# Performance work log

Measured on AMD Instinct MI355X. Metric: run time of the kernel, lower is better.

The kernel has to match this reference:

```python
import jax, jax.numpy as jnp
import numpy as np

B, T, D, NH, L = 8192, 100, 44, 64, 8  # batch, seq/ode steps, obs_dim, rnn hidden, latent


def setup_inputs() -> dict:
    key = jax.random.key(0)
    ks = jax.random.split(key, 12)
    s = 0.1
    return {
        "x": jax.random.normal(ks[0], (B, T, D), jnp.float32),
        "mask": jax.random.randint(ks[1], (B, T, D), 0, 2).astype(jnp.float32),
        "epsilon": jax.random.normal(ks[2], (B, L), jnp.float32),
        "Wi2h": jax.random.normal(ks[3], (D + NH, NH), jnp.float32) * s,
        "bi2h": jnp.zeros((NH,), jnp.float32),
        "Wh2o": jax.random.normal(ks[4], (NH, 2 * L), jnp.float32) * s,
        "bh2o": jnp.zeros((2 * L,), jnp.float32),
        "Wf1": jax.random.normal(ks[5], (L, NH), jnp.float32) * s,
        "bf1": jnp.zeros((NH,), jnp.float32),
        "Wf2": jax.random.normal(ks[6], (NH, NH), jnp.float32) * s,
        "bf2": jnp.zeros((NH,), jnp.float32),
        "Wf3": jax.random.normal(ks[7], (NH, L), jnp.float32) * s,
        "bf3": jnp.zeros((L,), jnp.float32),
        "Wd1": jax.random.normal(ks[8], (L, NH), jnp.float32) * s,
        "bd1": jnp.zeros((NH,), jnp.float32),
        "Wd2": jax.random.normal(ks[9], (NH, D), jnp.float32) * s,
        "bd2": jnp.zeros((D,), jnp.float32),
    }


def reference(x, mask, epsilon, Wi2h, bi2h, Wh2o, bh2o,
              Wf1, bf1, Wf2, bf2, Wf3, bf3, Wd1, bd1, Wd2, bd2):
    masked_x = x * mask  # [B,T,D]

    # --- reverse-time recognition RNN (scan over time, reversed) ---
    def rnn_step(h, obs):
        h = jnp.tanh(jnp.concatenate([obs, h], axis=1) @ Wi2h + bi2h)
        return h, None

    xs_rev = jnp.transpose(masked_x[:, ::-1, :], (1, 0, 2))  # [T,B,D]
    h0 = jnp.zeros((x.shape[0], Wi2h.shape[1]), x.dtype)
    h_final, _ = jax.lax.scan(rnn_step, h0, xs_rev)
    out = h_final @ Wh2o + bh2o  # [B,2L]
    qz0_mean, qz0_logvar = out[:, :L], out[:, L:]

    # reparameterized latent sample
    z0 = epsilon * jnp.exp(0.5 * qz0_logvar) + qz0_mean  # [B,L]

    # --- latent ODE dynamics, fixed-step RK4 over ts = linspace(0,1,100) ---
    def f(z):
        h1 = jax.nn.elu(z @ Wf1 + bf1)
        h2 = jax.nn.elu(h1 @ Wf2 + bf2)
        return h2 @ Wf3 + bf3

    dt = jnp.asarray(1.0 / (T - 1), x.dtype)

    def rk4_step(z, _):
        k1 = f(z)
        k2 = f(z + 0.5 * dt * k1)
        k3 = f(z + 0.5 * dt * k2)
        k4 = f(z + dt * k3)
        zn = z + (dt / 6.0) * (k1 + 2.0 * k2 + 2.0 * k3 + k4)
        return zn, zn

    _, zs = jax.lax.scan(rk4_step, z0, None, length=T - 1)  # [T-1,B,L]
    pred_z = jnp.transpose(jnp.concatenate([z0[None], zs], axis=0), (1, 0, 2))  # [B,T,L]

    # --- decoder ---
    pred_x = jax.nn.relu(pred_z @ Wd1 + bd1) @ Wd2 + bd2  # [B,T,D]

    # fill observed entries back in
    updated_x = jnp.where(masked_x != 0, masked_x, pred_x)

    # --- loss ---
    noise_logvar = 2.0 * jnp.log(jnp.asarray(0.3, x.dtype))
    log2pi = jnp.log(jnp.asarray(2.0 * np.pi, x.dtype))
    logpx = (-0.5 * (log2pi + noise_logvar +
                     (x - updated_x) ** 2 / jnp.exp(noise_logvar))).sum((-1, -2))  # [B]
    kl = (-0.5 * qz0_logvar + (jnp.exp(qz0_logvar) + qz0_mean ** 2) / 2.0 - 0.5).sum(-1)  # [B]
    loss = jnp.mean(-logpx + kl)
    return loss
```

## Files before the change

kernel.cpp:

```cpp
#include <hip/hip_runtime.h>
#include <stdint.h>


constexpr int B_ = 8192, T_ = 100, D_ = 44, NH_ = 64, L_ = 8;

typedef __bf16 bf16x8 __attribute__((ext_vector_type(8)));
typedef float f32x4 __attribute__((ext_vector_type(4)));
typedef uint32_t u32x4 __attribute__((ext_vector_type(4)));
typedef uint32_t u32x2 __attribute__((ext_vector_type(2)));

__device__ __forceinline__ float fexp2(float x) { return __builtin_amdgcn_exp2f(x); }
__device__ __forceinline__ float frcp(float x) { return __builtin_amdgcn_rcpf(x); }
__device__ __forceinline__ float fexp(float x) { return fexp2(x * 1.44269504088896341f); }
__device__ __forceinline__ float tanh_f(float x) {
  float e = fexp2(x * 2.88539008177792681f);
  return 1.0f - 2.0f * frcp(e + 1.0f);
}
__device__ __forceinline__ float elu_f(float x) { return x > 0.0f ? x : (fexp(x) - 1.0f); }
__device__ __forceinline__ uint32_t f2bs(float x) {
  return (uint32_t)__builtin_bit_cast(unsigned short, (__bf16)x);
}
__device__ __forceinline__ uint32_t pk(float lo, float hi) { return f2bs(lo) | (f2bs(hi) << 16); }
__device__ __forceinline__ uint32_t sh(uint32_t v, int s) { return (uint32_t)__shfl((int)v, s, 64); }
__device__ __forceinline__ f32x4 mfma16(bf16x8 a, bf16x8 b, f32x4 c) {
  return __builtin_amdgcn_mfma_f32_16x16x32_bf16(a, b, c, 0, 0, 0);
}
__device__ __forceinline__ bf16x8 pack8(float a, float b, float c, float d,
                                        float e, float f, float g, float h) {
  u32x4 u = {pk(a, b), pk(c, d), pk(e, f), pk(g, h)};
  return __builtin_bit_cast(bf16x8, u);
}
__device__ __forceinline__ float f4get(const float4& f, int i) {
  return i == 0 ? f.x : (i == 1 ? f.y : (i == 2 ? f.z : f.w));
}

__device__ __forceinline__ void repack_lds(uint32_t* tb, int c, int q,
                                           const f32x4* e, bf16x8* bh) {
#pragma unroll
  for (int tau = 0; tau < 4; ++tau) {
    u32x2 w = {pk(e[tau][0], e[tau][1]), pk(e[tau][2], e[tau][3])};
    *(u32x2*)(tb + 36 * c + 8 * tau + 2 * q) = w;
  }
#pragma unroll
  for (int ks = 0; ks < 2; ++ks) {
    u32x4 r = *(const u32x4*)(tb + 36 * c + 16 * ks + 4 * q);
    bh[ks] = __builtin_bit_cast(bf16x8, r);
  }
}

__device__ __forceinline__ bf16x8 build_bz(f32x4 z, int c, int q) {
  uint32_t p01 = pk(z[0], z[1]), p23 = pk(z[2], z[3]);
  u32x4 u = {sh(p01, c), sh(p23, c), sh(p01, c + 16), sh(p23, c + 16)};
  if (q == 1) u[0] = 0x3f80u;
  return __builtin_bit_cast(bf16x8, u);
}

__global__ __launch_bounds__(64) void fused_kernel(
    const float* __restrict__ x, const float* __restrict__ mask,
    const float* __restrict__ eps,
    const float* __restrict__ Wi2h, const float* __restrict__ bi2h,
    const float* __restrict__ Wh2o, const float* __restrict__ bh2o,
    const float* __restrict__ Wf1, const float* __restrict__ bf1,
    const float* __restrict__ Wf2, const float* __restrict__ bf2,
    const float* __restrict__ Wf3, const float* __restrict__ bf3,
    const float* __restrict__ Wd1, const float* __restrict__ bd1,
    const float* __restrict__ Wd2, const float* __restrict__ bd2,
    float* __restrict__ part) {
  const int lane = threadIdx.x;
  const int c = lane & 15, q = lane >> 4;
  const int r0 = blockIdx.x * 16;

  __shared__ uint32_t tbufA[576];
  __shared__ uint32_t tbufB[576];

  bf16x8 Ai[4][4];
#pragma unroll
  for (int tau = 0; tau < 4; ++tau)
#pragma unroll
    for (int ks = 0; ks < 4; ++ks) {
      bf16x8 f;
      const int m = 16 * tau + c;
#pragma unroll
      for (int i = 0; i < 8; ++i) {
        const int k = 32 * ks + 8 * q + i;
        float v = 0.0f;
        if (k < 64) v = Wi2h[(44 + k) * 64 + m];
        else if (k < 108) v = Wi2h[(k - 64) * 64 + m];
        else if (k == 108) v = bi2h[m];
        f[i] = (__bf16)v;
      }
      Ai[tau][ks] = f;
    }
  bf16x8 Ah2o[2];
#pragma unroll
  for (int ks = 0; ks < 2; ++ks) {
    bf16x8 f;
#pragma unroll
    for (int i = 0; i < 8; ++i) f[i] = (__bf16)Wh2o[(32 * ks + 8 * q + i) * 16 + c];
    Ah2o[ks] = f;
  }
  f32x4 bo;
#pragma unroll
  for (int r = 0; r < 4; ++r) bo[r] = bh2o[4 * q + r];

  const float* xrowbase = x + (size_t)(r0 + c) * T_ * D_;
  const float* mrowbase = mask + (size_t)(r0 + c) * T_ * D_;

  auto load_obs = [&](int t, float4& a0, float4& a1, float4& b0, float4& b1,
                      float4& ma0, float4& ma1, float4& mb0, float4& mb1) {
    const float4* xr = (const float4*)(xrowbase + (size_t)t * D_);
    const float4* mr = (const float4*)(mrowbase + (size_t)t * D_);
    a0 = xr[2 * q]; a1 = xr[2 * q + 1]; ma0 = mr[2 * q]; ma1 = mr[2 * q + 1];
    float4 zz = {0.f, 0.f, 0.f, 0.f};
    b0 = zz; b1 = zz; mb0 = zz; mb1 = zz;
    if (q == 0) { b0 = xr[8]; b1 = xr[9]; mb0 = mr[8]; mb1 = mr[9]; }
    else if (q == 1) { b0 = xr[10]; mb0 = mr[10]; }
  };

  f32x4 hc[4] = {};
  float4 a0, a1, b0, b1, ma0, ma1, mb0, mb1;
  load_obs(T_ - 1, a0, a1, b0, b1, ma0, ma1, mb0, mb1);

#pragma unroll 1
  for (int s = 0; s < T_; ++s) {
    const int t = T_ - 1 - s;
    float4 ca0 = a0, ca1 = a1, cb0 = b0, cb1 = b1;
    float4 cm0 = ma0, cm1 = ma1, cn0 = mb0, cn1 = mb1;
    if (t > 0) load_obs(t - 1, a0, a1, b0, b1, ma0, ma1, mb0, mb1);

    bf16x8 bh[2];
    repack_lds(tbufA, c, q, hc, bh);
    bf16x8 o2 = pack8(ca0.x * cm0.x, ca0.y * cm0.y, ca0.z * cm0.z, ca0.w * cm0.w,
                      ca1.x * cm1.x, ca1.y * cm1.y, ca1.z * cm1.z, ca1.w * cm1.w);
    const float e44 = (q == 1) ? 1.0f : cb1.x * cn1.x;
    bf16x8 o3 = pack8(cb0.x * cn0.x, cb0.y * cn0.y, cb0.z * cn0.z, cb0.w * cn0.w,
                      e44, cb1.y * cn1.y, cb1.z * cn1.z, cb1.w * cn1.w);
#pragma unroll
    for (int tau = 0; tau < 4; ++tau) {
      f32x4 zero = {0.f, 0.f, 0.f, 0.f};
      f32x4 acc = mfma16(Ai[tau][0], bh[0], zero);
      acc = mfma16(Ai[tau][1], bh[1], acc);
      acc = mfma16(Ai[tau][2], o2, acc);
      acc = mfma16(Ai[tau][3], o3, acc);
#pragma unroll
      for (int r = 0; r < 4; ++r) hc[tau][r] = tanh_f(acc[r]);
    }
  }

  bf16x8 bhF[2];
  repack_lds(tbufA, c, q, hc, bhF);
  f32x4 o = mfma16(Ah2o[1], bhF[1], mfma16(Ah2o[0], bhF[0], bo));

  float lv[4];
#pragma unroll
  for (int r = 0; r < 4; ++r)
    lv[r] = __int_as_float(__shfl(__float_as_int(o[r]), lane + 32, 64));

  float klt = 0.0f;
  f32x4 z = {};
  if (q < 2) {
    const float4 ev = *(const float4*)(eps + (size_t)(r0 + c) * 8 + 4 * q);
#pragma unroll
    for (int r = 0; r < 4; ++r) {
      const float m = o[r];
      z[r] = f4get(ev, r) * fexp(0.5f * lv[r]) + m;
      klt += -0.5f * lv[r] + (fexp(lv[r]) + m * m) * 0.5f - 0.5f;
    }
  }
  klt += __shfl_xor(klt, 1);  klt += __shfl_xor(klt, 2);
  klt += __shfl_xor(klt, 4);  klt += __shfl_xor(klt, 8);
  klt += __shfl_xor(klt, 16); klt += __shfl_xor(klt, 32);

  __builtin_amdgcn_sched_barrier(0);

  bf16x8 A1[4], A2[4][2], A3[2], Ad1[4], Ad2[3][2];
#pragma unroll
  for (int tau = 0; tau < 4; ++tau) {
    bf16x8 f1, fd;
#pragma unroll
    for (int i = 0; i < 8; ++i) {
      const int k = 8 * q + i;
      f1[i] = (__bf16)(k < 8 ? Wf1[k * 64 + 16 * tau + c] : (k == 8 ? bf1[16 * tau + c] : 0.0f));
      fd[i] = (__bf16)(k < 8 ? Wd1[k * 64 + 16 * tau + c] : (k == 8 ? bd1[16 * tau + c] : 0.0f));
    }
    A1[tau] = f1; Ad1[tau] = fd;
#pragma unroll
    for (int ks = 0; ks < 2; ++ks) {
      bf16x8 g;
#pragma unroll
      for (int i = 0; i < 8; ++i) g[i] = (__bf16)Wf2[(32 * ks + 8 * q + i) * 64 + 16 * tau + c];
      A2[tau][ks] = g;
    }
  }
#pragma unroll
  for (int ks = 0; ks < 2; ++ks) {
    bf16x8 f;
#pragma unroll
    for (int i = 0; i < 8; ++i)
      f[i] = (__bf16)((c < 8) ? Wf3[(32 * ks + 8 * q + i) * 8 + c] : 0.0f);
    A3[ks] = f;
  }
#pragma unroll
  for (int tau = 0; tau < 3; ++tau)
#pragma unroll
    for (int ks = 0; ks < 2; ++ks) {
      bf16x8 f;
      const int m = 16 * tau + c;
#pragma unroll
      for (int i = 0; i < 8; ++i)
        f[i] = (__bf16)((m < 44) ? Wd2[(32 * ks + 8 * q + i) * 44 + m] : 0.0f);
      Ad2[tau][ks] = f;
    }
  f32x4 b2_[4], b3_, bd2_[3];
#pragma unroll
  for (int tau = 0; tau < 4; ++tau)
#pragma unroll
    for (int r = 0; r < 4; ++r) b2_[tau][r] = bf2[16 * tau + 4 * q + r];
#pragma unroll
  for (int r = 0; r < 4; ++r) b3_[r] = (q < 2) ? bf3[4 * q + r] : 0.0f;
#pragma unroll
  for (int tau = 0; tau < 3; ++tau)
#pragma unroll
    for (int r = 0; r < 4; ++r) {
      const int d = 16 * tau + 4 * q + r;
      bd2_[tau][r] = (d < 44) ? bd2[d] : 0.0f;
    }

  auto feval = [&](bf16x8 bz) -> f32x4 {
    f32x4 h[4];
#pragma unroll
    for (int tau = 0; tau < 4; ++tau) {
      f32x4 zero = {0.f, 0.f, 0.f, 0.f};
      h[tau] = mfma16(A1[tau], bz, zero);
#pragma unroll
      for (int r = 0; r < 4; ++r) h[tau][r] = elu_f(h[tau][r]);
    }
    bf16x8 bh[2];
    repack_lds(tbufA, c, q, h, bh);
    f32x4 g[4];
#pragma unroll
    for (int tau = 0; tau < 4; ++tau) {
      g[tau] = mfma16(A2[tau][1], bh[1], mfma16(A2[tau][0], bh[0], b2_[tau]));
#pragma unroll
      for (int r = 0; r < 4; ++r) g[tau][r] = elu_f(g[tau][r]);
    }
    bf16x8 bg[2];
    repack_lds(tbufA, c, q, g, bg);
    return mfma16(A3[1], bg[1], mfma16(A3[0], bg[0], b3_));
  };

  auto load_xm = [&](int t, float4* xv, float4* mv) {
#pragma unroll
    for (int tau = 0; tau < 3; ++tau) {
      const int d0 = 16 * tau + 4 * q;
      if (d0 < 44) {
        const size_t off = (size_t)(r0 + c) * T_ * D_ + (size_t)t * D_ + d0;
        xv[tau] = *(const float4*)(x + off);
        mv[tau] = *(const float4*)(mask + off);
      }
    }
  };

  const float dt = 1.0f / (float)(T_ - 1);
  const float hdt = 0.5f * dt;
  float qacc = 0.0f;

  float4 xc[3], mc[3], xn[3], mn[3];
  load_xm(0, xc, mc);

#pragma unroll 1
  for (int t = 0; t < T_; ++t) {
    if (t < T_ - 1) load_xm(t + 1, xn, mn);

    bf16x8 bz = build_bz(z, c, q);

    f32x4 hd[4];
#pragma unroll
    for (int tau = 0; tau < 4; ++tau) {
      f32x4 zero = {0.f, 0.f, 0.f, 0.f};
      hd[tau] = mfma16(Ad1[tau], bz, zero);
#pragma unroll
      for (int r = 0; r < 4; ++r) hd[tau][r] = fmaxf(hd[tau][r], 0.0f);
    }
    bf16x8 bhd[2];
    repack_lds(tbufB, c, q, hd, bhd);
#pragma unroll
    for (int tau = 0; tau < 3; ++tau) {
      f32x4 p = mfma16(Ad2[tau][1], bhd[1], mfma16(Ad2[tau][0], bhd[0], bd2_[tau]));
      if (16 * tau + 4 * q < 44) {
#pragma unroll
        for (int r = 0; r < 4; ++r) {
          const float xa = f4get(xc[tau], r), ma = f4get(mc[tau], r);
          const float mx = xa * ma;
          const float upd = (mx != 0.0f) ? mx : p[r];
          const float df = xa - upd;
          qacc += df * df;
        }
      }
    }

    if (t < T_ - 1) {
      f32x4 k1 = feval(bz);
      f32x4 zt;
#pragma unroll
      for (int r = 0; r < 4; ++r) zt[r] = z[r] + hdt * k1[r];
      f32x4 k2 = feval(build_bz(zt, c, q));
#pragma unroll
      for (int r = 0; r < 4; ++r) zt[r] = z[r] + hdt * k2[r];
      f32x4 k3 = feval(build_bz(zt, c, q));
#pragma unroll
      for (int r = 0; r < 4; ++r) zt[r] = z[r] + dt * k3[r];
      f32x4 k4 = feval(build_bz(zt, c, q));
#pragma unroll
      for (int r = 0; r < 4; ++r)
        z[r] += (dt / 6.0f) * (k1[r] + 2.0f * (k2[r] + k3[r]) + k4[r]);
#pragma unroll
      for (int tau = 0; tau < 3; ++tau) { xc[tau] = xn[tau]; mc[tau] = mn[tau]; }
    }
  }

  float tot = qacc * (0.5f / 0.09f);
  tot += __shfl_xor(tot, 1);  tot += __shfl_xor(tot, 2);
  tot += __shfl_xor(tot, 4);  tot += __shfl_xor(tot, 8);
  tot += __shfl_xor(tot, 16); tot += __shfl_xor(tot, 32);
  if (lane == 0) part[blockIdx.x] = tot + klt;
}

__global__ __launch_bounds__(512) void reduce_kernel(const float* __restrict__ part,
                                                     float* __restrict__ out) {
  __shared__ float s[8];
  const int tid = threadIdx.x;
  float v = part[tid];
  v += __shfl_xor(v, 1);  v += __shfl_xor(v, 2);
  v += __shfl_xor(v, 4);  v += __shfl_xor(v, 8);
  v += __shfl_xor(v, 16); v += __shfl_xor(v, 32);
  if ((tid & 63) == 0) s[tid >> 6] = v;
  __syncthreads();
  if (tid == 0) {
    float acc = 0.0f;
#pragma unroll
    for (int i = 0; i < 8; ++i) acc += s[i];
    const float c0 = 0.28503427112126353f;
    out[0] = acc * (1.0f / (float)B_) - (float)(T_ * D_) * c0;
  }
}

extern "C" void kernel_launch(void* const* d_in, const int* in_sizes, int n_in,
                              void* d_out, int out_size, void* d_ws, size_t ws_size,
                              hipStream_t stream) {
  const float* x    = (const float*)d_in[0];
  const float* mask = (const float*)d_in[1];
  const float* eps  = (const float*)d_in[2];
  const float* Wi2h = (const float*)d_in[3];
  const float* bi2h = (const float*)d_in[4];
  const float* Wh2o = (const float*)d_in[5];
  const float* bh2o = (const float*)d_in[6];
  const float* Wf1  = (const float*)d_in[7];
  const float* bf1  = (const float*)d_in[8];
  const float* Wf2  = (const float*)d_in[9];
  const float* bf2  = (const float*)d_in[10];
  const float* Wf3  = (const float*)d_in[11];
  const float* bf3  = (const float*)d_in[12];
  const float* Wd1  = (const float*)d_in[13];
  const float* bd1  = (const float*)d_in[14];
  const float* Wd2  = (const float*)d_in[15];
  const float* bd2  = (const float*)d_in[16];

  float* loss = (float*)d_out;
  float* part = (float*)d_ws;

  fused_kernel<<<dim3(B_ / 16), dim3(64), 0, stream>>>(
      x, mask, eps, Wi2h, bi2h, Wh2o, bh2o, Wf1, bf1, Wf2, bf2, Wf3, bf3,
      Wd1, bd1, Wd2, bd2, part);
  reduce_kernel<<<dim3(1), dim3(512), 0, stream>>>(part, loss);
}
```

Measured before the change: 825.2 us.

## Process two batch tiles per wave to interleave independent MFMA chains

Each 64-lane wave now handles two 16-row batch tiles, interleaving their RNN, RK4 and decoder MFMA/transcendental chains to hide dependency latency. Observation loads are packed one step ahead, and the decoder loss is computed after the RK4 step reusing the same latent operand. The grid is halved and the final reduction shrinks to match. Risks include higher register pressure, possible spills, and fewer waves across CUs.

```diff
diff --git a/kernel.cpp b/kernel.cpp
--- a/kernel.cpp
+++ b/kernel.cpp
@@ -3,6 +3,7 @@
 
 
 constexpr int B_ = 8192, T_ = 100, D_ = 44, NH_ = 64, L_ = 8;
+constexpr int NT = 2;
 
 typedef __bf16 bf16x8 __attribute__((ext_vector_type(8)));
 typedef float f32x4 __attribute__((ext_vector_type(4)));
@@ -34,20 +35,6 @@
   return i == 0 ? f.x : (i == 1 ? f.y : (i == 2 ? f.z : f.w));
 }
 
-__device__ __forceinline__ void repack_lds(uint32_t* tb, int c, int q,
-                                           const f32x4* e, bf16x8* bh) {
-#pragma unroll
-  for (int tau = 0; tau < 4; ++tau) {
-    u32x2 w = {pk(e[tau][0], e[tau][1]), pk(e[tau][2], e[tau][3])};
-    *(u32x2*)(tb + 36 * c + 8 * tau + 2 * q) = w;
-  }
-#pragma unroll
-  for (int ks = 0; ks < 2; ++ks) {
-    u32x4 r = *(const u32x4*)(tb + 36 * c + 16 * ks + 4 * q);
-    bh[ks] = __builtin_bit_cast(bf16x8, r);
-  }
-}
-
 __device__ __forceinline__ bf16x8 build_bz(f32x4 z, int c, int q) {
   uint32_t p01 = pk(z[0], z[1]), p23 = pk(z[2], z[3]);
   u32x4 u = {sh(p01, c), sh(p23, c), sh(p01, c + 16), sh(p23, c + 16)};
@@ -55,7 +42,7 @@
   return __builtin_bit_cast(bf16x8, u);
 }
 
-__global__ __launch_bounds__(64) void fused_kernel(
+__global__ __launch_bounds__(64, 1) void fused_kernel(
     const float* __restrict__ x, const float* __restrict__ mask,
     const float* __restrict__ eps,
     const float* __restrict__ Wi2h, const float* __restrict__ bi2h,
@@ -68,10 +55,26 @@
     float* __restrict__ part) {
   const int lane = threadIdx.x;
   const int c = lane & 15, q = lane >> 4;
-  const int r0 = blockIdx.x * 16;
-
-  __shared__ uint32_t tbufA[576];
-  __shared__ uint32_t tbufB[576];
+  const int r0 = blockIdx.x * (16 * NT);
+
+  __shared__ uint32_t tbuf[NT][576];
+
+  auto repack2 = [&](const f32x4 (*e)[4], bf16x8 (*bh)[2]) {
+#pragma unroll
+    for (int nt = 0; nt < NT; ++nt)
+#pragma unroll
+      for (int tau = 0; tau < 4; ++tau) {
+        u32x2 w = {pk(e[nt][tau][0], e[nt][tau][1]), pk(e[nt][tau][2], e[nt][tau][3])};
+        *(u32x2*)(&tbuf[nt][0] + 36 * c + 8 * tau + 2 * q) = w;
+      }
+#pragma unroll
+    for (int nt = 0; nt < NT; ++nt)
+#pragma unroll
+      for (int ks = 0; ks < 2; ++ks) {
+        u32x4 r = *(const u32x4*)(&tbuf[nt][0] + 36 * c + 16 * ks + 4 * q);
+        bh[nt][ks] = __builtin_bit_cast(bf16x8, r);
+      }
+  };
 
   bf16x8 Ai[4][4];
 #pragma unroll
@@ -103,73 +106,90 @@
 #pragma unroll
   for (int r = 0; r < 4; ++r) bo[r] = bh2o[4 * q + r];
 
-  const float* xrowbase = x + (size_t)(r0 + c) * T_ * D_;
-  const float* mrowbase = mask + (size_t)(r0 + c) * T_ * D_;
-
-  auto load_obs = [&](int t, float4& a0, float4& a1, float4& b0, float4& b1,
-                      float4& ma0, float4& ma1, float4& mb0, float4& mb1) {
-    const float4* xr = (const float4*)(xrowbase + (size_t)t * D_);
-    const float4* mr = (const float4*)(mrowbase + (size_t)t * D_);
-    a0 = xr[2 * q]; a1 = xr[2 * q + 1]; ma0 = mr[2 * q]; ma1 = mr[2 * q + 1];
-    float4 zz = {0.f, 0.f, 0.f, 0.f};
-    b0 = zz; b1 = zz; mb0 = zz; mb1 = zz;
-    if (q == 0) { b0 = xr[8]; b1 = xr[9]; mb0 = mr[8]; mb1 = mr[9]; }
-    else if (q == 1) { b0 = xr[10]; mb0 = mr[10]; }
+  const float* xrow0 = x + (size_t)(r0 + c) * T_ * D_;
+  const float* mrow0 = mask + (size_t)(r0 + c) * T_ * D_;
+  const float* xrow1 = x + (size_t)(r0 + 16 + c) * T_ * D_;
+  const float* mrow1 = mask + (size_t)(r0 + 16 + c) * T_ * D_;
+
+  float4 rx[NT][4], rm[NT][4];
+  bf16x8 po2[NT], po3[NT];
+
+  auto issue_obs = [&](int t) {
+#pragma unroll
+    for (int nt = 0; nt < NT; ++nt) {
+      const float4* xr = (const float4*)((nt ? xrow1 : xrow0) + (size_t)t * D_);
+      const float4* mr = (const float4*)((nt ? mrow1 : mrow0) + (size_t)t * D_);
+      rx[nt][0] = xr[2 * q];     rx[nt][1] = xr[2 * q + 1];
+      rm[nt][0] = mr[2 * q];     rm[nt][1] = mr[2 * q + 1];
+      float4 zz = {0.f, 0.f, 0.f, 0.f};
+      rx[nt][2] = zz; rx[nt][3] = zz; rm[nt][2] = zz; rm[nt][3] = zz;
+      if (q == 0) { rx[nt][2] = xr[8];  rx[nt][3] = xr[9];
+                    rm[nt][2] = mr[8];  rm[nt][3] = mr[9]; }
+      else if (q == 1) { rx[nt][2] = xr[10]; rm[nt][2] = mr[10]; }
+    }
   };
-
-  f32x4 hc[4] = {};
-  float4 a0, a1, b0, b1, ma0, ma1, mb0, mb1;
-  load_obs(T_ - 1, a0, a1, b0, b1, ma0, ma1, mb0, mb1);
+  auto pack_obs = [&]() {
+#pragma unroll
+    for (int nt = 0; nt < NT; ++nt) {
+      const float4 A0 = rx[nt][0], A1 = rx[nt][1], B0 = rx[nt][2], B1 = rx[nt][3];
+      const float4 M0 = rm[nt][0], M1 = rm[nt][1], N0 = rm[nt][2], N1 = rm[nt][3];
+      po2[nt] = pack8(A0.x * M0.x, A0.y * M0.y, A0.z * M0.z, A0.w * M0.w,
+                      A1.x * M1.x, A1.y * M1.y, A1.z * M1.z, A1.w * M1.w);
+      const float e44 = (q == 1) ? 1.0f : B1.x * N1.x;
+      po3[nt] = pack8(B0.x * N0.x, B0.y * N0.y, B0.z * N0.z, B0.w * N0.w,
+                      e44, B1.y * N1.y, B1.z * N1.z, B1.w * N1.w);
+    }
+  };
+
+  f32x4 hc[NT][4] = {};
+  issue_obs(T_ - 1);
+  pack_obs();
 
 #pragma unroll 1
   for (int s = 0; s < T_; ++s) {
     const int t = T_ - 1 - s;
-    float4 ca0 = a0, ca1 = a1, cb0 = b0, cb1 = b1;
-    float4 cm0 = ma0, cm1 = ma1, cn0 = mb0, cn1 = mb1;
-    if (t > 0) load_obs(t - 1, a0, a1, b0, b1, ma0, ma1, mb0, mb1);
-
-    bf16x8 bh[2];
-    repack_lds(tbufA, c, q, hc, bh);
-    bf16x8 o2 = pack8(ca0.x * cm0.x, ca0.y * cm0.y, ca0.z * cm0.z, ca0.w * cm0.w,
-                      ca1.x * cm1.x, ca1.y * cm1.y, ca1.z * cm1.z, ca1.w * cm1.w);
-    const float e44 = (q == 1) ? 1.0f : cb1.x * cn1.x;
-    bf16x8 o3 = pack8(cb0.x * cn0.x, cb0.y * cn0.y, cb0.z * cn0.z, cb0.w * cn0.w,
-                      e44, cb1.y * cn1.y, cb1.z * cn1.z, cb1.w * cn1.w);
-#pragma unroll
-    for (int tau = 0; tau < 4; ++tau) {
-      f32x4 zero = {0.f, 0.f, 0.f, 0.f};
-      f32x4 acc = mfma16(Ai[tau][0], bh[0], zero);
-      acc = mfma16(Ai[tau][1], bh[1], acc);
-      acc = mfma16(Ai[tau][2], o2, acc);
-      acc = mfma16(Ai[tau][3], o3, acc);
-#pragma unroll
-      for (int r = 0; r < 4; ++r) hc[tau][r] = tanh_f(acc[r]);
-    }
-  }
-
-  bf16x8 bhF[2];
-  repack_lds(tbufA, c, q, hc, bhF);
-  f32x4 o = mfma16(Ah2o[1], bhF[1], mfma16(Ah2o[0], bhF[0], bo));
-
-  float lv[4];
-#pragma unroll
-  for (int r = 0; r < 4; ++r)
-    lv[r] = __int_as_float(__shfl(__float_as_int(o[r]), lane + 32, 64));
-
+    if (t > 0) issue_obs(t - 1);
+
+    bf16x8 bh[NT][2];
+    repack2(hc, bh);
+#pragma unroll
+    for (int nt = 0; nt < NT; ++nt)
+#pragma unroll
+      for (int tau = 0; tau < 4; ++tau) {
+        f32x4 acc = {0.f, 0.f, 0.f, 0.f};
+        acc = mfma16(Ai[tau][0], bh[nt][0], acc);
+        acc = mfma16(Ai[tau][1], bh[nt][1], acc);
+        acc = mfma16(Ai[tau][2], po2[nt], acc);
+        acc = mfma16(Ai[tau][3], po3[nt], acc);
+#pragma unroll
+        for (int r = 0; r < 4; ++r) hc[nt][tau][r] = tanh_f(acc[r]);
+      }
+    if (t > 0) pack_obs();
+  }
+
+  bf16x8 bhF[NT][2];
+  repack2(hc, bhF);
   float klt = 0.0f;
-  f32x4 z = {};
-  if (q < 2) {
-    const float4 ev = *(const float4*)(eps + (size_t)(r0 + c) * 8 + 4 * q);
-#pragma unroll
-    for (int r = 0; r < 4; ++r) {
-      const float m = o[r];
-      z[r] = f4get(ev, r) * fexp(0.5f * lv[r]) + m;
-      klt += -0.5f * lv[r] + (fexp(lv[r]) + m * m) * 0.5f - 0.5f;
-    }
-  }
-  klt += __shfl_xor(klt, 1);  klt += __shfl_xor(klt, 2);
-  klt += __shfl_xor(klt, 4);  klt += __shfl_xor(klt, 8);
-  klt += __shfl_xor(klt, 16); klt += __shfl_xor(klt, 32);
+  f32x4 z[NT];
+#pragma unroll
+  for (int nt = 0; nt < NT; ++nt) {
+    f32x4 o = mfma16(Ah2o[1], bhF[nt][1], mfma16(Ah2o[0], bhF[nt][0], bo));
+    float lv[4];
+#pragma unroll
+    for (int r = 0; r < 4; ++r)
+      lv[r] = __int_as_float(__shfl(__float_as_int(o[r]), lane + 32, 64));
+    f32x4 zz = {0.f, 0.f, 0.f, 0.f};
+    z[nt] = zz;
+    if (q < 2) {
+      const float4 ev = *(const float4*)(eps + (size_t)(r0 + 16 * nt + c) * 8 + 4 * q);
+#pragma unroll
+      for (int r = 0; r < 4; ++r) {
+        const float m = o[r];
+        z[nt][r] = f4get(ev, r) * fexp(0.5f * lv[r]) + m;
+        klt += -0.5f * lv[r] + (fexp(lv[r]) + m * m) * 0.5f - 0.5f;
+      }
+    }
+  }
 
   __builtin_amdgcn_sched_barrier(0);
 
@@ -226,109 +246,137 @@
       bd2_[tau][r] = (d < 44) ? bd2[d] : 0.0f;
     }
 
-  auto feval = [&](bf16x8 bz) -> f32x4 {
-    f32x4 h[4];
-#pragma unroll
-    for (int tau = 0; tau < 4; ++tau) {
-      f32x4 zero = {0.f, 0.f, 0.f, 0.f};
-      h[tau] = mfma16(A1[tau], bz, zero);
-#pragma unroll
-      for (int r = 0; r < 4; ++r) h[tau][r] = elu_f(h[tau][r]);
-    }
-    bf16x8 bh[2];
-    repack_lds(tbufA, c, q, h, bh);
-    f32x4 g[4];
-#pragma unroll
-    for (int tau = 0; tau < 4; ++tau) {
-      g[tau] = mfma16(A2[tau][1], bh[1], mfma16(A2[tau][0], bh[0], b2_[tau]));
-#pragma unroll
-      for (int r = 0; r < 4; ++r) g[tau][r] = elu_f(g[tau][r]);
-    }
-    bf16x8 bg[2];
-    repack_lds(tbufA, c, q, g, bg);
-    return mfma16(A3[1], bg[1], mfma16(A3[0], bg[0], b3_));
-  };
-
-  auto load_xm = [&](int t, float4* xv, float4* mv) {
-#pragma unroll
-    for (int tau = 0; tau < 3; ++tau) {
-      const int d0 = 16 * tau + 4 * q;
-      if (d0 < 44) {
-        const size_t off = (size_t)(r0 + c) * T_ * D_ + (size_t)t * D_ + d0;
-        xv[tau] = *(const float4*)(x + off);
-        mv[tau] = *(const float4*)(mask + off);
-      }
-    }
+  auto feval2 = [&](const bf16x8* bz, f32x4* kout) {
+    f32x4 h[NT][4];
+#pragma unroll
+    for (int nt = 0; nt < NT; ++nt)
+#pragma unroll
+      for (int tau = 0; tau < 4; ++tau) {
+        f32x4 zero = {0.f, 0.f, 0.f, 0.f};
+        h[nt][tau] = mfma16(A1[tau], bz[nt], zero);
+#pragma unroll
+        for (int r = 0; r < 4; ++r) h[nt][tau][r] = elu_f(h[nt][tau][r]);
+      }
+    bf16x8 bh[NT][2];
+    repack2(h, bh);
+    f32x4 g[NT][4];
+#pragma unroll
+    for (int nt = 0; nt < NT; ++nt)
+#pragma unroll
+      for (int tau = 0; tau < 4; ++tau) {
+        g[nt][tau] = mfma16(A2[tau][1], bh[nt][1], mfma16(A2[tau][0], bh[nt][0], b2_[tau]));
+#pragma unroll
+        for (int r = 0; r < 4; ++r) g[nt][tau][r] = elu_f(g[nt][tau][r]);
+      }
+    bf16x8 bg[NT][2];
+    repack2(g, bg);
+#pragma unroll
+    for (int nt = 0; nt < NT; ++nt)
+      kout[nt] = mfma16(A3[1], bg[nt][1], mfma16(A3[0], bg[nt][0], b3_));
   };
 
   const float dt = 1.0f / (float)(T_ - 1);
   const float hdt = 0.5f * dt;
   float qacc = 0.0f;
 
-  float4 xc[3], mc[3], xn[3], mn[3];
-  load_xm(0, xc, mc);
-
 #pragma unroll 1
   for (int t = 0; t < T_; ++t) {
-    if (t < T_ - 1) load_xm(t + 1, xn, mn);
-
-    bf16x8 bz = build_bz(z, c, q);
-
-    f32x4 hd[4];
-#pragma unroll
-    for (int tau = 0; tau < 4; ++tau) {
-      f32x4 zero = {0.f, 0.f, 0.f, 0.f};
-      hd[tau] = mfma16(Ad1[tau], bz, zero);
-#pragma unroll
-      for (int r = 0; r < 4; ++r) hd[tau][r] = fmaxf(hd[tau][r], 0.0f);
-    }
-    bf16x8 bhd[2];
-    repack_lds(tbufB, c, q, hd, bhd);
-#pragma unroll
-    for (int tau = 0; tau < 3; ++tau) {
-      f32x4 p = mfma16(Ad2[tau][1], bhd[1], mfma16(Ad2[tau][0], bhd[0], bd2_[tau]));
-      if (16 * tau + 4 * q < 44) {
+    float4 xc[NT][3], mc[NT][3];
+#pragma unroll
+    for (int nt = 0; nt < NT; ++nt)
+#pragma unroll
+      for (int tau = 0; tau < 3; ++tau) {
+        const int d0 = 16 * tau + 4 * q;
+        if (d0 < 44) {
+          const size_t off = (size_t)(r0 + 16 * nt + c) * T_ * D_ + (size_t)t * D_ + d0;
+          xc[nt][tau] = *(const float4*)(x + off);
+          mc[nt][tau] = *(const float4*)(mask + off);
+        }
+      }
+
+    bf16x8 bzd[NT];
+#pragma unroll
+    for (int nt = 0; nt < NT; ++nt) bzd[nt] = build_bz(z[nt], c, q);
+
+    if (t < T_ - 1) {
+      f32x4 kacc[NT], kc[NT], zt[NT];
+      bf16x8 bzt[NT];
+      feval2(bzd, kc);
+#pragma unroll
+      for (int nt = 0; nt < NT; ++nt) {
+        kacc[nt] = kc[nt];
+#pragma unroll
+        for (int r = 0; r < 4; ++r) zt[nt][r] = z[nt][r] + hdt * kc[nt][r];
+        bzt[nt] = build_bz(zt[nt], c, q);
+      }
+      feval2(bzt, kc);
+#pragma unroll
+      for (int nt = 0; nt < NT; ++nt) {
 #pragma unroll
         for (int r = 0; r < 4; ++r) {
-          const float xa = f4get(xc[tau], r), ma = f4get(mc[tau], r);
-          const float mx = xa * ma;
-          const float upd = (mx != 0.0f) ? mx : p[r];
-          const float df = xa - upd;
-          qacc += df * df;
+          kacc[nt][r] += 2.0f * kc[nt][r];
+          zt[nt][r] = z[nt][r] + hdt * kc[nt][r];
         }
-      }
-    }
-
-    if (t < T_ - 1) {
-      f32x4 k1 = feval(bz);
-      f32x4 zt;
-#pragma unroll
-      for (int r = 0; r < 4; ++r) zt[r] = z[r] + hdt * k1[r];
-      f32x4 k2 = feval(build_bz(zt, c, q));
-#pragma unroll
-      for (int r = 0; r < 4; ++r) zt[r] = z[r] + hdt * k2[r];
-      f32x4 k3 = feval(build_bz(zt, c, q));
-#pragma unroll
-      for (int r = 0; r < 4; ++r) zt[r] = z[r] + dt * k3[r];
-      f32x4 k4 = feval(build_bz(zt, c, q));
-#pragma unroll
-      for (int r = 0; r < 4; ++r)
-        z[r] += (dt / 6.0f) * (k1[r] + 2.0f * (k2[r] + k3[r]) + k4[r]);
-#pragma unroll
-      for (int tau = 0; tau < 3; ++tau) { xc[tau] = xn[tau]; mc[tau] = mn[tau]; }
-    }
-  }
-
-  float tot = qacc * (0.5f / 0.09f);
+        bzt[nt] = build_bz(zt[nt], c, q);
+      }
+      feval2(bzt, kc);
+#pragma unroll
+      for (int nt = 0; nt < NT; ++nt) {
+#pragma unroll
+        for (int r = 0; r < 4; ++r) {
+          kacc[nt][r] += 2.0f * kc[nt][r];
+          zt[nt][r] = z[nt][r] + dt * kc[nt][r];
+        }
+        bzt[nt] = build_bz(zt[nt], c, q);
+      }
+      feval2(bzt, kc);
+#pragma unroll
+      for (int nt = 0; nt < NT; ++nt)
+#pragma unroll
+        for (int r = 0; r < 4; ++r)
+          z[nt][r] += (dt / 6.0f) * (kacc[nt][r] + kc[nt][r]);
+    }
+
+    f32x4 hd[NT][4];
+#pragma unroll
+    for (int nt = 0; nt < NT; ++nt)
+#pragma unroll
+      for (int tau = 0; tau < 4; ++tau) {
+        f32x4 zero = {0.f, 0.f, 0.f, 0.f};
+        hd[nt][tau] = mfma16(Ad1[tau], bzd[nt], zero);
+#pragma unroll
+        for (int r = 0; r < 4; ++r) hd[nt][tau][r] = fmaxf(hd[nt][tau][r], 0.0f);
+      }
+    bf16x8 bhd[NT][2];
+    repack2(hd, bhd);
+#pragma unroll
+    for (int nt = 0; nt < NT; ++nt)
+#pragma unroll
+      for (int tau = 0; tau < 3; ++tau) {
+        f32x4 p = mfma16(Ad2[tau][1], bhd[nt][1], mfma16(Ad2[tau][0], bhd[nt][0], bd2_[tau]));
+        if (16 * tau + 4 * q < 44) {
+#pragma unroll
+          for (int r = 0; r < 4; ++r) {
+            const float xa = f4get(xc[nt][tau], r), ma = f4get(mc[nt][tau], r);
+            const float mx = xa * ma;
+            const float upd = (mx != 0.0f) ? mx : p[r];
+            const float df = xa - upd;
+            qacc += df * df;
+          }
+        }
+      }
+  }
+
+  float tot = qacc * (0.5f / 0.09f) + klt;
   tot += __shfl_xor(tot, 1);  tot += __shfl_xor(tot, 2);
   tot += __shfl_xor(tot, 4);  tot += __shfl_xor(tot, 8);
   tot += __shfl_xor(tot, 16); tot += __shfl_xor(tot, 32);
-  if (lane == 0) part[blockIdx.x] = tot + klt;
-}
-
-__global__ __launch_bounds__(512) void reduce_kernel(const float* __restrict__ part,
+  if (lane == 0) part[blockIdx.x] = tot;
+}
+
+__global__ __launch_bounds__(256) void reduce_kernel(const float* __restrict__ part,
                                                      float* __restrict__ out) {
-  __shared__ float s[8];
+  __shared__ float s[4];
   const int tid = threadIdx.x;
   float v = part[tid];
   v += __shfl_xor(v, 1);  v += __shfl_xor(v, 2);
@@ -337,9 +385,7 @@
   if ((tid & 63) == 0) s[tid >> 6] = v;
   __syncthreads();
   if (tid == 0) {
-    float acc = 0.0f;
-#pragma unroll
-    for (int i = 0; i < 8; ++i) acc += s[i];
+    float acc = s[0] + s[1] + s[2] + s[3];
     const float c0 = 0.28503427112126353f;
     out[0] = acc * (1.0f / (float)B_) - (float)(T_ * D_) * c0;
   }
@@ -369,8 +415,8 @@
   float* loss = (float*)d_out;
   float* part = (float*)d_ws;
 
-  fused_kernel<<<dim3(B_ / 16), dim3(64), 0, stream>>>(
+  fused_kernel<<<dim3(B_ / (16 * NT)), dim3(64), 0, stream>>>(
       x, mask, eps, Wi2h, bi2h, Wh2o, bh2o, Wf1, bf1, Wf2, bf2, Wf3, bf3,
       Wd1, bd1, Wd2, bd2, part);
-  reduce_kernel<<<dim3(1), dim3(512), 0, stream>>>(part, loss);
-}
+  reduce_kernel<<<dim3(1), dim3(256), 0, stream>>>(part, loss);
+}
```

Result: slower. 1.312 ms (+58.9%).
